# Performance work log

Hardware: AMD Instinct MI355X
Metric: run time of the kernel (lower is better)

Reference implementation:

```python
import jax, jax.numpy as jnp
import numpy as np

DIM = 256
N_PATCHES = 2048
N_HEADS = 8
BATCH = 2


def setup_inputs() -> dict:
    key = jax.random.key(0)
    ks = jax.random.split(key, 8)
    d = DIM
    s = d ** -0.5
    return {
        "x": jax.random.normal(ks[0], (BATCH, N_PATCHES, d), dtype=jnp.float32),
        # weights stored (in_features, out_features) so y = x @ W + b
        "W_qk": jax.random.normal(ks[1], (d, 2 * d), dtype=jnp.float32) * s,
        "W_v": jax.random.normal(ks[2], (d, d), dtype=jnp.float32) * s,
        "W_proj": jax.random.normal(ks[3], (d, d), dtype=jnp.float32) * s,
        "b_proj": jnp.zeros((d,), dtype=jnp.float32),
        "W_pos": jax.random.normal(ks[4], (2, N_HEADS), dtype=jnp.float32) * 0.5,
        "b_pos": jnp.zeros((N_HEADS,), dtype=jnp.float32),
        "gating": jnp.ones((N_HEADS,), dtype=jnp.float32),
    }


def reference(x, W_qk, W_v, W_proj, b_proj, W_pos, b_pos, gating):
    B, N, C = x.shape
    H = gating.shape[0]
    Dh = C // H
    scale = Dh ** -0.5

    # content attention: q @ k^T softmax
    qk = (x @ W_qk).reshape(B, N, 2, H, Dh)
    q = jnp.transpose(qk[:, :, 0], (0, 2, 1, 3))  # [B,H,N,Dh]
    k = jnp.transpose(qk[:, :, 1], (0, 2, 1, 3))
    patch_score = jax.nn.softmax(jnp.einsum("bhnd,bhmd->bhnm", q, k) * scale, axis=-1)

    # positional attention from relative indices (d, |d|) -> per-head score
    idx = jnp.arange(N, dtype=jnp.float32)
    rel = idx[:, None] - idx[None, :]                      # [N,N]
    rel_feat = jnp.stack([rel, jnp.abs(rel)], axis=-1)     # [N,N,2]
    pos = rel_feat @ W_pos + b_pos                         # [N,N,H]
    pos_score = jax.nn.softmax(jnp.transpose(pos, (2, 0, 1)), axis=-1)  # [H,N,N]

    g = jax.nn.sigmoid(gating)[None, :, None, None]        # [1,H,1,1]
    attn = (1.0 - g) * patch_score + g * pos_score[None]   # [B,H,N,N]
    attn = attn / jnp.sum(attn, axis=-1, keepdims=True)

    v = jnp.transpose((x @ W_v).reshape(B, N, H, Dh), (0, 2, 1, 3))  # [B,H,N,Dh]
    out = jnp.einsum("bhnm,bhmd->bhnd", attn, v)
    out = jnp.transpose(out, (0, 2, 1, 3)).reshape(B, N, C)
    return out @ W_proj + b_proj
```

## Files before the change

kernel.cpp:

```cpp
#include <hip/hip_runtime.h>
#include <hip/hip_bf16.h>

#define DIM 256
#define NP 2048
#define NH 8
#define BATCH 2
#define DH 32

typedef __attribute__((ext_vector_type(8))) short bshort8;
typedef __attribute__((ext_vector_type(4))) short bshort4;
typedef __attribute__((ext_vector_type(4))) float f32x4;

#define LOG2E 1.44269504f
#define QSCALE (0.17677669529663687f * LOG2E)

union U16B { uint4 u; bshort8 s8; bshort4 s4x[2]; __hip_bfloat16 h[8]; };
union U8B  { uint2 u; bshort4 s4; __hip_bfloat16 h[4]; };

__device__ __forceinline__ float fexp2(float x) { return __builtin_amdgcn_exp2f(x); }
__device__ __forceinline__ unsigned packbf(float hi, float lo) {
    return __builtin_amdgcn_perm(__float_as_uint(hi), __float_as_uint(lo), 0x07060302u);
}

__device__ __forceinline__ int lds_addr(int row, int colg) {
    return row * 256 + (((colg ^ (row & 7)) & 31) << 3);
}

__device__ __forceinline__ void gl16(const void* g, void* l) {
    __builtin_amdgcn_global_load_lds(
        (const __attribute__((address_space(1))) void*)g,
        (__attribute__((address_space(3))) void*)l, 16, 0, 0);
}

__global__ __launch_bounds__(256) void prep_kernel(
    const float* __restrict__ Wqk,
    const float* __restrict__ Wv,
    const float* __restrict__ Wproj,
    const float* __restrict__ x,
    __hip_bfloat16* __restrict__ WT,
    __hip_bfloat16* __restrict__ xb) {
    const int t = threadIdx.x;
    const int blk = blockIdx.x;
    if (blk >= 64) {
        const int base = (blk - 64) * 256 + t;
#pragma unroll
        for (int i = 0; i < 16; i++) {
            const int idx = base + i * 16384;
            float4 f = *(const float4*)(x + (size_t)idx * 4);
            U8B a;
            a.h[0] = __float2bfloat16(f.x); a.h[1] = __float2bfloat16(f.y);
            a.h[2] = __float2bfloat16(f.z); a.h[3] = __float2bfloat16(f.w);
            *(uint2*)(xb + (size_t)idx * 4) = a.u;
        }
        return;
    }
    __shared__ float ts[64][65];
    const int ct = blk >> 2, k0 = (blk & 3) * 64;
    const int c0 = ct * 64;
    const float* src; int ldw, cs0; float scl = 1.0f;
    if (ct < 8)       { src = Wqk;   ldw = 512; cs0 = c0;      if (ct < 4) scl = QSCALE; }
    else if (ct < 12) { src = Wv;    ldw = 256; cs0 = c0 - 512; }
    else              { src = Wproj; ldw = 256; cs0 = c0 - 768; }
    const int cc = t & 63, tq = t >> 6;
#pragma unroll
    for (int j = 0; j < 16; j++) {
        int kk = tq * 16 + j;
        ts[kk][cc] = src[(size_t)(k0 + kk) * ldw + cs0 + cc];
    }
    __syncthreads();
    const int kk2 = t & 63;
#pragma unroll
    for (int j = 0; j < 16; j++) {
        int cc2 = tq * 16 + j;
        WT[(size_t)(c0 + cc2) * 256 + k0 + kk2] = __float2bfloat16(ts[kk2][cc2] * scl);
    }
}

__global__ __launch_bounds__(256) void qkv_mfma(
    const __hip_bfloat16* __restrict__ xb,
    const __hip_bfloat16* __restrict__ WT,
    __hip_bfloat16* __restrict__ qT,
    __hip_bfloat16* __restrict__ k,
    __hip_bfloat16* __restrict__ vT) {
    __shared__ __align__(16) __hip_bfloat16 As[64 * 256];
    __shared__ __align__(16) __hip_bfloat16 Bs[64 * 256];
    const int t = threadIdx.x, lane = t & 63, wvid = t >> 6;
    const int l15 = lane & 15, l4 = lane >> 4;
    const int m0 = blockIdx.x * 64;
    const int nb0 = blockIdx.y * 64;
    const int nc = nb0 + wvid * 16 + l15;

    const int lrow = lane >> 5, lcg = lane & 31;
#pragma unroll
    for (int j = 0; j < 8; j++) {
        const int r0 = j * 8 + wvid * 2;
        const int row = r0 + lrow;
        const int cgs = (lcg ^ (row & 7)) & 31;
        gl16(xb + (((size_t)(m0 + row)) << 8) + cgs * 8, (char*)As + r0 * 512);
        gl16(WT + (((size_t)(nb0 + row)) << 8) + cgs * 8, (char*)Bs + r0 * 512);
    }
    __syncthreads();

    f32x4 acc[4] = {{0.f,0.f,0.f,0.f},{0.f,0.f,0.f,0.f},{0.f,0.f,0.f,0.f},{0.f,0.f,0.f,0.f}};
#pragma unroll
    for (int kk = 0; kk < 8; kk++) {
        const int colg = kk * 4 + l4;
        U16B bw; bw.u = *(const uint4*)&Bs[lds_addr(wvid * 16 + l15, colg)];
#pragma unroll
        for (int mt = 0; mt < 4; mt++) {
            U16B ax; ax.u = *(const uint4*)&As[lds_addr(mt * 16 + l15, colg)];
            acc[mt] = __builtin_amdgcn_mfma_f32_16x16x32_bf16(ax.s8, bw.s8, acc[mt], 0, 0, 0);
        }
    }

    if (nb0 < 256) {
        const int c = nc;
        const int b = m0 >> 11;
#pragma unroll
        for (int mt = 0; mt < 4; mt++) {
            int tokn = (m0 & (NP - 1)) + mt * 16 + l4 * 4;
            U8B vv;
#pragma unroll
            for (int r = 0; r < 4; r++) vv.h[r] = __float2bfloat16(acc[mt][r]);
            *(uint2*)(qT + (size_t)(b * 256 + c) * NP + tokn) = vv.u;
        }
    } else if (nb0 < 512) {
        const int c = nc - 256, h = c >> 5, d = c & 31;
#pragma unroll
        for (int mt = 0; mt < 4; mt++)
#pragma unroll
            for (int r = 0; r < 4; r++) {
                int tok = m0 + mt * 16 + l4 * 4 + r;
                int b = tok >> 11, n = tok & (NP - 1);
                k[((size_t)(b * NH + h) * NP + n) * DH + d] = __float2bfloat16(acc[mt][r]);
            }
    } else {
        const int c = nc - 512;
        const int b = m0 >> 11;
#pragma unroll
        for (int mt = 0; mt < 4; mt++) {
            int tokn = (m0 & (NP - 1)) + mt * 16 + l4 * 4;
            U8B vv;
#pragma unroll
            for (int r = 0; r < 4; r++) vv.h[r] = __float2bfloat16(acc[mt][r]);
            *(uint2*)(vT + (size_t)(b * 256 + c) * NP + tokn) = vv.u;
        }
    }
}

__global__ __launch_bounds__(512, 4) void attn_kernel(
    const __hip_bfloat16* __restrict__ qg,
    const __hip_bfloat16* __restrict__ kg,
    const __hip_bfloat16* __restrict__ vTg,
    const float* __restrict__ Wpos,
    const float* __restrict__ bpos,
    const float* __restrict__ gating,
    __hip_bfloat16* __restrict__ ao) {
    __shared__ __align__(16) __hip_bfloat16 Kt[2][2][64][40];
    __shared__ __align__(16) __hip_bfloat16 Vt[2][2][32][72];
    __shared__ float cmb[4][2][32][16];
    __shared__ float cls[4][2][16];

    const int t = threadIdx.x;
    const int lane = t & 63, wvid = t >> 6;
    const int l15 = lane & 15, l4 = lane >> 4;
    const int qt = wvid & 3, kh = wvid >> 2;
    const int bh = blockIdx.x >> 5, qb = blockIdx.x & 31;
    const int h = bh & (NH - 1), b = bh >> 3;
    const int q0 = qb * 64 + qt * 16;
    const int myq = q0 + l15;

    const int st_ = t & 255;
    const int kstart = kh * 1024;
    const __hip_bfloat16* kptr = kg + (size_t)bh * NP * DH + (size_t)(kstart + (st_ >> 2)) * DH + (st_ & 3) * 8;
    const __hip_bfloat16* vptr = vTg + ((size_t)bh * DH + (st_ >> 3)) * NP + kstart + (st_ & 7) * 8;

    const int vd = st_ >> 3, vs = st_ & 7;
    const int vc0 = ((2 * vs) & 3) * 16 + (vs >> 1) * 4;
    const int vc1 = ((2 * vs + 1) & 3) * 16 + (vs >> 1) * 4;

    uint4 kreg = *(const uint4*)kptr;
    uint4 vreg = *(const uint4*)vptr;
    *(uint4*)&Kt[kh][0][st_ >> 2][(st_ & 3) * 8] = kreg;
    *(uint2*)&Vt[kh][0][vd][vc0] = make_uint2(vreg.x, vreg.y);
    *(uint2*)&Vt[kh][0][vd][vc1] = make_uint2(vreg.z, vreg.w);

    const float w0 = Wpos[h] * LOG2E;
    const float w1 = Wpos[NH + h] * LOG2E;
    const float g = 1.0f / (1.0f + __expf(-gating[h]));
    const float nf = (float)myq;
    const float pmax = fmaxf(0.f, fmaxf((w0 + w1) * nf, (w1 - w0) * (2047.0f - nf)));
    const float npmax = -pmax;
    const float rA = fexp2(-(w0 + w1));
    const float rB = fexp2(w1 - w0);

    U16B qv;
#pragma unroll
    for (int j = 0; j < 8; j++)
        qv.h[j] = qg[((size_t)bh * DH + l4 * 8 + j) * NP + myq];

    __syncthreads();

    f32x4 os0 = {0.f,0.f,0.f,0.f}, os1 = {0.f,0.f,0.f,0.f};
    f32x4 op0 = {0.f,0.f,0.f,0.f}, op1 = {0.f,0.f,0.f,0.f};
    float ls = 0.f, lp = 0.f;

    for (int it = 0; it < 16; ++it) {
        const int cur = it & 1, nxt = cur ^ 1;

        if (it < 15) {
            kreg = *(const uint4*)(kptr + (size_t)(it + 1) * 64 * DH);
            vreg = *(const uint4*)(vptr + (it + 1) * 64);
        }

        f32x4 st4[4];
#pragma unroll
        for (int kt = 0; kt < 4; kt++) {
            U16B kf; kf.u = *(const uint4*)&Kt[kh][cur][kt * 16 + l15][l4 * 8];
            st4[kt] = __builtin_amdgcn_mfma_f32_16x16x32_bf16(
                kf.s8, qv.s8, (f32x4){0.f,0.f,0.f,0.f}, 0, 0, 0);
        }

        U16B va0, va1, vb0, vb1;
        {
            const __hip_bfloat16* v0 = &Vt[kh][cur][l15][l4 * 16];
            const __hip_bfloat16* v1 = &Vt[kh][cur][16 + l15][l4 * 16];
            va0.u = *(const uint4*)v0;
            va1.u = *(const uint4*)(v0 + 8);
            vb0.u = *(const uint4*)v1;
            vb1.u = *(const uint4*)(v1 + 8);
        }

        const int kb0 = kstart + it * 64;
#pragma unroll
        for (int kt = 0; kt < 4; kt++) {
            const bshort4 fa = (kt < 2) ? va0.s4x[kt & 1] : va1.s4x[kt & 1];
            const bshort4 fb = (kt < 2) ? vb0.s4x[kt & 1] : vb1.s4x[kt & 1];
            float es0 = fexp2(st4[kt][0]), es1 = fexp2(st4[kt][1]);
            float es2 = fexp2(st4[kt][2]), es3 = fexp2(st4[kt][3]);
            ls += (es0 + es1) + (es2 + es3);
            const float d0 = nf - (float)(kb0 + kt * 16 + l4 * 4);
            float ep0 = fexp2(fmaf(w1, fabsf(d0), fmaf(w0, d0, npmax)));
            float ep1 = ep0 * ((d0 >= 1.f) ? rA : rB);
            float ep2 = ep1 * ((d0 >= 2.f) ? rA : rB);
            float ep3 = ep2 * ((d0 >= 3.f) ? rA : rB);
            lp += (ep0 + ep1) + (ep2 + ep3);
            U8B pc, pp;
            pc.u.x = packbf(es1, es0); pc.u.y = packbf(es3, es2);
            pp.u.x = packbf(ep1, ep0); pp.u.y = packbf(ep3, ep2);
            os0 = __builtin_amdgcn_mfma_f32_16x16x16bf16_1k(fa, pc.s4, os0, 0, 0, 0);
            os1 = __builtin_amdgcn_mfma_f32_16x16x16bf16_1k(fb, pc.s4, os1, 0, 0, 0);
            op0 = __builtin_amdgcn_mfma_f32_16x16x16bf16_1k(fa, pp.s4, op0, 0, 0, 0);
            op1 = __builtin_amdgcn_mfma_f32_16x16x16bf16_1k(fb, pp.s4, op1, 0, 0, 0);
        }

        if (it < 15) {
            *(uint4*)&Kt[kh][nxt][st_ >> 2][(st_ & 3) * 8] = kreg;
            *(uint2*)&Vt[kh][nxt][vd][vc0] = make_uint2(vreg.x, vreg.y);
            *(uint2*)&Vt[kh][nxt][vd][vc1] = make_uint2(vreg.z, vreg.w);
        }
        __syncthreads();
    }

    ls += __shfl_xor(ls, 16, 64); ls += __shfl_xor(ls, 32, 64);
    lp += __shfl_xor(lp, 16, 64); lp += __shfl_xor(lp, 32, 64);

    if (kh == 1) {
#pragma unroll
        for (int r = 0; r < 4; r++) {
            cmb[qt][0][l4 * 4 + r][l15]      = os0[r];
            cmb[qt][0][16 + l4 * 4 + r][l15] = os1[r];
            cmb[qt][1][l4 * 4 + r][l15]      = op0[r];
            cmb[qt][1][16 + l4 * 4 + r][l15] = op1[r];
        }
        if (l4 == 0) { cls[qt][0][l15] = ls; cls[qt][1][l15] = lp; }
    }
    __syncthreads();
    if (kh == 0) {
        ls += cls[qt][0][l15]; lp += cls[qt][1][l15];
        const float cs = (1.0f - g) / ls;
        const float cp = g / lp;
        const size_t orow = ((size_t)b * NP + myq) * DIM + h * DH;
        U8B o0, o1;
#pragma unroll
        for (int r = 0; r < 4; r++) {
            o0.h[r] = __float2bfloat16(cs * (os0[r] + cmb[qt][0][l4 * 4 + r][l15]) +
                                       cp * (op0[r] + cmb[qt][1][l4 * 4 + r][l15]));
            o1.h[r] = __float2bfloat16(cs * (os1[r] + cmb[qt][0][16 + l4 * 4 + r][l15]) +
                                       cp * (op1[r] + cmb[qt][1][16 + l4 * 4 + r][l15]));
        }
        *(uint2*)(ao + orow + l4 * 4)      = o0.u;
        *(uint2*)(ao + orow + 16 + l4 * 4) = o1.u;
    }
}

__global__ __launch_bounds__(256) void proj_mfma(
    const __hip_bfloat16* __restrict__ ao,
    const __hip_bfloat16* __restrict__ WT,
    const float* __restrict__ bias,
    float* __restrict__ out) {
    __shared__ __align__(16) __hip_bfloat16 As[64 * 256];
    __shared__ __align__(16) __hip_bfloat16 Bs[64 * 256];
    const int t = threadIdx.x, lane = t & 63, wvid = t >> 6;
    const int l15 = lane & 15, l4 = lane >> 4;
    const int m0 = blockIdx.x * 64;
    const int nb0 = blockIdx.y * 64;
    const int nc = nb0 + wvid * 16 + l15;

    const int lrow = lane >> 5, lcg = lane & 31;
#pragma unroll
    for (int j = 0; j < 8; j++) {
        const int r0 = j * 8 + wvid * 2;
        const int row = r0 + lrow;
        const int cgs = (lcg ^ (row & 7)) & 31;
        gl16(ao + (((size_t)(m0 + row)) << 8) + cgs * 8, (char*)As + r0 * 512);
        gl16(WT + (((size_t)(768 + nb0 + row)) << 8) + cgs * 8, (char*)Bs + r0 * 512);
    }
    __syncthreads();

    f32x4 acc[4] = {{0.f,0.f,0.f,0.f},{0.f,0.f,0.f,0.f},{0.f,0.f,0.f,0.f},{0.f,0.f,0.f,0.f}};
#pragma unroll
    for (int kk = 0; kk < 8; kk++) {
        const int colg = kk * 4 + l4;
        U16B bw; bw.u = *(const uint4*)&Bs[lds_addr(wvid * 16 + l15, colg)];
#pragma unroll
        for (int mt = 0; mt < 4; mt++) {
            U16B ax; ax.u = *(const uint4*)&As[lds_addr(mt * 16 + l15, colg)];
            acc[mt] = __builtin_amdgcn_mfma_f32_16x16x32_bf16(ax.s8, bw.s8, acc[mt], 0, 0, 0);
        }
    }

    const float bb = bias[nc];
#pragma unroll
    for (int mt = 0; mt < 4; mt++)
#pragma unroll
        for (int r = 0; r < 4; r++) {
            int tok = m0 + mt * 16 + l4 * 4 + r;
            out[(size_t)tok * 256 + nc] = acc[mt][r] + bb;
        }
}

extern "C" void kernel_launch(void* const* d_in, const int* in_sizes, int n_in,
                              void* d_out, int out_size, void* d_ws, size_t ws_size,
                              hipStream_t stream) {
    const float* x      = (const float*)d_in[0];
    const float* Wqk    = (const float*)d_in[1];
    const float* Wv     = (const float*)d_in[2];
    const float* Wproj  = (const float*)d_in[3];
    const float* bproj  = (const float*)d_in[4];
    const float* Wpos   = (const float*)d_in[5];
    const float* bpos   = (const float*)d_in[6];
    const float* gating = (const float*)d_in[7];
    float* out = (float*)d_out;

    const size_t nElem = (size_t)BATCH * NP * DIM;
    char* w = (char*)d_ws;
    __hip_bfloat16* WT = (__hip_bfloat16*)w;
    __hip_bfloat16* qT = WT + 262144;
    __hip_bfloat16* k  = qT + nElem;
    __hip_bfloat16* vT = k + nElem;
    __hip_bfloat16* ao = vT + nElem;
    __hip_bfloat16* xb = ao + nElem;

    prep_kernel<<<128, 256, 0, stream>>>(Wqk, Wv, Wproj, x, WT, xb);
    qkv_mfma<<<dim3(64, 12), 256, 0, stream>>>(xb, WT, qT, k, vT);
    attn_kernel<<<BATCH * NH * (NP / 64), 512, 0, stream>>>(qT, k, vT, Wpos, bpos, gating, ao);
    proj_mfma<<<dim3(64, 4), 256, 0, stream>>>(ao, WT, bproj, out);
}
```

Measured before the change: 107.8 us.

## Fuse all four stages into one persistent kernel with grid-wide barriers

Replaces the prep, QKV GEMM, attention and projection launches with a single 512-block kernel that separates the stages using atomic-counter grid barriers, reusing one shared-memory buffer across stages. The QKV and projection GEMMs are re-tiled to 64x128 outputs with two K-chunks to fit the shared budget. This targets launch gaps and tail effects between kernels. The cost is spin-wait barrier overhead, a required memset, idle blocks during the small GEMM stages, and a deadlock risk if all 512 blocks cannot be co-resident.

```diff
diff --git a/kernel.cpp b/kernel.cpp
--- a/kernel.cpp
+++ b/kernel.cpp
@@ -21,323 +21,327 @@
 __device__ __forceinline__ unsigned packbf(float hi, float lo) {
     return __builtin_amdgcn_perm(__float_as_uint(hi), __float_as_uint(lo), 0x07060302u);
 }
-
-__device__ __forceinline__ int lds_addr(int row, int colg) {
-    return row * 256 + (((colg ^ (row & 7)) & 31) << 3);
-}
-
 __device__ __forceinline__ void gl16(const void* g, void* l) {
     __builtin_amdgcn_global_load_lds(
         (const __attribute__((address_space(1))) void*)g,
         (__attribute__((address_space(3))) void*)l, 16, 0, 0);
 }
-
-__global__ __launch_bounds__(256) void prep_kernel(
+__device__ __forceinline__ int lds_a(int row, int colg) {
+    return row * 128 + (((colg ^ (row & 7)) & 15) << 3);
+}
+
+__device__ __forceinline__ void gbar(unsigned* sem, unsigned target) {
+    __syncthreads();
+    if (threadIdx.x == 0) {
+        __threadfence();
+        __hip_atomic_fetch_add(sem, 1u, __ATOMIC_RELEASE, __HIP_MEMORY_SCOPE_AGENT);
+        while (__hip_atomic_load(sem, __ATOMIC_ACQUIRE, __HIP_MEMORY_SCOPE_AGENT) < target)
+            __builtin_amdgcn_s_sleep(8);
+        __threadfence();
+    }
+    __syncthreads();
+}
+
+struct QkvS {
+    __hip_bfloat16 As[64 * 128];
+    __hip_bfloat16 Bs[128 * 128];
+};
+struct AttnS {
+    __hip_bfloat16 Kt[2][2][64][40];
+    __hip_bfloat16 Vt[2][2][32][72];
+    float cmb[4][2][32][16];
+    float cls[4][2][16];
+};
+struct PrepS { float ts[64][65]; };
+
+__device__ __forceinline__ void gemm64x128(
+    const __hip_bfloat16* __restrict__ Ag, size_t arow0,
+    const __hip_bfloat16* __restrict__ Bg, size_t brow0,
+    QkvS& sq, int t, f32x4 acc[4])
+{
+    const int lane = t & 63, wvid = t >> 6;
+    const int l15 = lane & 15, l4 = lane >> 4;
+    const int lg = lane & 15, lr4 = lane >> 4;
+#pragma unroll
+    for (int kc = 0; kc < 2; kc++) {
+        if (kc) __syncthreads();
+#pragma unroll
+        for (int j = 0; j < 2; j++) {
+            int r = (j * 8 + wvid) * 4 + lr4;
+            int sg = lg ^ (r & 7);
+            gl16(Ag + ((arow0 + r) << 8) + kc * 128 + sg * 8,
+                 (char*)sq.As + (j * 8 + wvid) * 1024);
+        }
+#pragma unroll
+        for (int j = 0; j < 4; j++) {
+            int r = (j * 8 + wvid) * 4 + lr4;
+            int sg = lg ^ (r & 7);
+            gl16(Bg + ((brow0 + r) << 8) + kc * 128 + sg * 8,
+                 (char*)sq.Bs + (j * 8 + wvid) * 1024);
+        }
+        __syncthreads();
+#pragma unroll
+        for (int kk = 0; kk < 4; kk++) {
+            const int colg = kk * 4 + l4;
+            U16B bw; bw.u = *(const uint4*)&sq.Bs[lds_a(wvid * 16 + l15, colg)];
+#pragma unroll
+            for (int mt = 0; mt < 4; mt++) {
+                U16B ax; ax.u = *(const uint4*)&sq.As[lds_a(mt * 16 + l15, colg)];
+                acc[mt] = __builtin_amdgcn_mfma_f32_16x16x32_bf16(ax.s8, bw.s8, acc[mt], 0, 0, 0);
+            }
+        }
+    }
+}
+
+__global__ __launch_bounds__(512, 4) void fused_kernel(
+    const float* __restrict__ x,
     const float* __restrict__ Wqk,
     const float* __restrict__ Wv,
     const float* __restrict__ Wproj,
-    const float* __restrict__ x,
+    const float* __restrict__ bproj,
+    const float* __restrict__ Wpos,
+    const float* __restrict__ gating,
+    float* __restrict__ out,
     __hip_bfloat16* __restrict__ WT,
-    __hip_bfloat16* __restrict__ xb) {
+    __hip_bfloat16* __restrict__ xb,
+    __hip_bfloat16* __restrict__ qT,
+    __hip_bfloat16* __restrict__ kbuf,
+    __hip_bfloat16* __restrict__ vT,
+    __hip_bfloat16* __restrict__ ao,
+    unsigned* __restrict__ sems)
+{
+    __shared__ __align__(16) char smem[55808];
+
     const int t = threadIdx.x;
-    const int blk = blockIdx.x;
-    if (blk >= 64) {
-        const int base = (blk - 64) * 256 + t;
-#pragma unroll
-        for (int i = 0; i < 16; i++) {
-            const int idx = base + i * 16384;
+    const int bid = blockIdx.x;
+    const int lane = t & 63, wvid = t >> 6;
+    const int l15 = lane & 15, l4 = lane >> 4;
+
+    if (bid < 64) {
+        PrepS& sp = *(PrepS*)smem;
+        const int ct = bid >> 2, k0 = (bid & 3) * 64, c0 = ct * 64;
+        const float* src; int ldw, cs0; float scl = 1.0f;
+        if (ct < 8)       { src = Wqk;   ldw = 512; cs0 = c0;       if (ct < 4) scl = QSCALE; }
+        else if (ct < 12) { src = Wv;    ldw = 256; cs0 = c0 - 512; }
+        else              { src = Wproj; ldw = 256; cs0 = c0 - 768; }
+        const int cc = t & 63, tq = t >> 6;
+#pragma unroll
+        for (int j = 0; j < 8; j++) {
+            int kk = tq * 8 + j;
+            sp.ts[kk][cc] = src[(size_t)(k0 + kk) * ldw + cs0 + cc];
+        }
+        __syncthreads();
+        const int kk2 = t & 63;
+#pragma unroll
+        for (int j = 0; j < 8; j++) {
+            int cc2 = tq * 8 + j;
+            WT[(size_t)(c0 + cc2) * 256 + k0 + kk2] = __float2bfloat16(sp.ts[kk2][cc2] * scl);
+        }
+    } else {
+        const int base = (bid - 64) * 512 + t;
+        for (int idx = base; idx < 262144; idx += 229376) {
             float4 f = *(const float4*)(x + (size_t)idx * 4);
             U8B a;
             a.h[0] = __float2bfloat16(f.x); a.h[1] = __float2bfloat16(f.y);
             a.h[2] = __float2bfloat16(f.z); a.h[3] = __float2bfloat16(f.w);
             *(uint2*)(xb + (size_t)idx * 4) = a.u;
         }
-        return;
-    }
-    __shared__ float ts[64][65];
-    const int ct = blk >> 2, k0 = (blk & 3) * 64;
-    const int c0 = ct * 64;
-    const float* src; int ldw, cs0; float scl = 1.0f;
-    if (ct < 8)       { src = Wqk;   ldw = 512; cs0 = c0;      if (ct < 4) scl = QSCALE; }
-    else if (ct < 12) { src = Wv;    ldw = 256; cs0 = c0 - 512; }
-    else              { src = Wproj; ldw = 256; cs0 = c0 - 768; }
-    const int cc = t & 63, tq = t >> 6;
-#pragma unroll
-    for (int j = 0; j < 16; j++) {
-        int kk = tq * 16 + j;
-        ts[kk][cc] = src[(size_t)(k0 + kk) * ldw + cs0 + cc];
-    }
-    __syncthreads();
-    const int kk2 = t & 63;
-#pragma unroll
-    for (int j = 0; j < 16; j++) {
-        int cc2 = tq * 16 + j;
-        WT[(size_t)(c0 + cc2) * 256 + k0 + kk2] = __float2bfloat16(ts[kk2][cc2] * scl);
-    }
-}
-
-__global__ __launch_bounds__(256) void qkv_mfma(
-    const __hip_bfloat16* __restrict__ xb,
-    const __hip_bfloat16* __restrict__ WT,
-    __hip_bfloat16* __restrict__ qT,
-    __hip_bfloat16* __restrict__ k,
-    __hip_bfloat16* __restrict__ vT) {
-    __shared__ __align__(16) __hip_bfloat16 As[64 * 256];
-    __shared__ __align__(16) __hip_bfloat16 Bs[64 * 256];
-    const int t = threadIdx.x, lane = t & 63, wvid = t >> 6;
-    const int l15 = lane & 15, l4 = lane >> 4;
-    const int m0 = blockIdx.x * 64;
-    const int nb0 = blockIdx.y * 64;
-    const int nc = nb0 + wvid * 16 + l15;
-
-    const int lrow = lane >> 5, lcg = lane & 31;
-#pragma unroll
-    for (int j = 0; j < 8; j++) {
-        const int r0 = j * 8 + wvid * 2;
-        const int row = r0 + lrow;
-        const int cgs = (lcg ^ (row & 7)) & 31;
-        gl16(xb + (((size_t)(m0 + row)) << 8) + cgs * 8, (char*)As + r0 * 512);
-        gl16(WT + (((size_t)(nb0 + row)) << 8) + cgs * 8, (char*)Bs + r0 * 512);
-    }
-    __syncthreads();
-
-    f32x4 acc[4] = {{0.f,0.f,0.f,0.f},{0.f,0.f,0.f,0.f},{0.f,0.f,0.f,0.f},{0.f,0.f,0.f,0.f}};
-#pragma unroll
-    for (int kk = 0; kk < 8; kk++) {
-        const int colg = kk * 4 + l4;
-        U16B bw; bw.u = *(const uint4*)&Bs[lds_addr(wvid * 16 + l15, colg)];
-#pragma unroll
-        for (int mt = 0; mt < 4; mt++) {
-            U16B ax; ax.u = *(const uint4*)&As[lds_addr(mt * 16 + l15, colg)];
-            acc[mt] = __builtin_amdgcn_mfma_f32_16x16x32_bf16(ax.s8, bw.s8, acc[mt], 0, 0, 0);
-        }
-    }
-
-    if (nb0 < 256) {
-        const int c = nc;
-        const int b = m0 >> 11;
-#pragma unroll
-        for (int mt = 0; mt < 4; mt++) {
-            int tokn = (m0 & (NP - 1)) + mt * 16 + l4 * 4;
-            U8B vv;
-#pragma unroll
-            for (int r = 0; r < 4; r++) vv.h[r] = __float2bfloat16(acc[mt][r]);
-            *(uint2*)(qT + (size_t)(b * 256 + c) * NP + tokn) = vv.u;
-        }
-    } else if (nb0 < 512) {
-        const int c = nc - 256, h = c >> 5, d = c & 31;
+    }
+    gbar(sems + 0, 512);
+
+    if (bid < 384) {
+        QkvS& sq = *(QkvS*)smem;
+        const int ct2 = bid >> 6, rt = bid & 63;
+        const int m0 = rt * 64, nb0 = ct2 * 128;
+        f32x4 acc[4] = {{0.f,0.f,0.f,0.f},{0.f,0.f,0.f,0.f},{0.f,0.f,0.f,0.f},{0.f,0.f,0.f,0.f}};
+        gemm64x128(xb, (size_t)m0, WT, (size_t)nb0, sq, t, acc);
+
+        const int nc = nb0 + wvid * 16 + l15;
+        if (nc < 256) {
+            const int b = m0 >> 11;
+#pragma unroll
+            for (int mt = 0; mt < 4; mt++) {
+                int tokn = (m0 & (NP - 1)) + mt * 16 + l4 * 4;
+                U8B vv;
+#pragma unroll
+                for (int r = 0; r < 4; r++) vv.h[r] = __float2bfloat16(acc[mt][r]);
+                *(uint2*)(qT + (size_t)(b * 256 + nc) * NP + tokn) = vv.u;
+            }
+        } else if (nc < 512) {
+            const int c = nc - 256, h = c >> 5, d = c & 31;
+#pragma unroll
+            for (int mt = 0; mt < 4; mt++)
+#pragma unroll
+                for (int r = 0; r < 4; r++) {
+                    int tok = m0 + mt * 16 + l4 * 4 + r;
+                    int b = tok >> 11, n = tok & (NP - 1);
+                    kbuf[((size_t)(b * NH + h) * NP + n) * DH + d] = __float2bfloat16(acc[mt][r]);
+                }
+        } else {
+            const int c = nc - 512;
+            const int b = m0 >> 11;
+#pragma unroll
+            for (int mt = 0; mt < 4; mt++) {
+                int tokn = (m0 & (NP - 1)) + mt * 16 + l4 * 4;
+                U8B vv;
+#pragma unroll
+                for (int r = 0; r < 4; r++) vv.h[r] = __float2bfloat16(acc[mt][r]);
+                *(uint2*)(vT + (size_t)(b * 256 + c) * NP + tokn) = vv.u;
+            }
+        }
+    }
+    gbar(sems + 1, 512);
+
+    {
+        AttnS& sa = *(AttnS*)smem;
+        const int qt = wvid & 3, kh = wvid >> 2;
+        const int bh = bid >> 5, qb = bid & 31;
+        const int h = bh & (NH - 1), b = bh >> 3;
+        const int q0 = qb * 64 + qt * 16;
+        const int myq = q0 + l15;
+
+        const int st_ = t & 255;
+        const int kstart = kh * 1024;
+        const __hip_bfloat16* kptr = kbuf + (size_t)bh * NP * DH + (size_t)(kstart + (st_ >> 2)) * DH + (st_ & 3) * 8;
+        const __hip_bfloat16* vptr = vT + ((size_t)bh * DH + (st_ >> 3)) * NP + kstart + (st_ & 7) * 8;
+
+        const int vd = st_ >> 3, vs = st_ & 7;
+        const int vc0 = ((2 * vs) & 3) * 16 + (vs >> 1) * 4;
+        const int vc1 = ((2 * vs + 1) & 3) * 16 + (vs >> 1) * 4;
+
+        uint4 kreg = *(const uint4*)kptr;
+        uint4 vreg = *(const uint4*)vptr;
+        *(uint4*)&sa.Kt[kh][0][st_ >> 2][(st_ & 3) * 8] = kreg;
+        *(uint2*)&sa.Vt[kh][0][vd][vc0] = make_uint2(vreg.x, vreg.y);
+        *(uint2*)&sa.Vt[kh][0][vd][vc1] = make_uint2(vreg.z, vreg.w);
+
+        const float w0 = Wpos[h] * LOG2E;
+        const float w1 = Wpos[NH + h] * LOG2E;
+        const float g = 1.0f / (1.0f + __expf(-gating[h]));
+        const float nf = (float)myq;
+        const float pmax = fmaxf(0.f, fmaxf((w0 + w1) * nf, (w1 - w0) * (2047.0f - nf)));
+        const float npmax = -pmax;
+        const float rA = fexp2(-(w0 + w1));
+        const float rB = fexp2(w1 - w0);
+
+        U16B qv;
+#pragma unroll
+        for (int j = 0; j < 8; j++)
+            qv.h[j] = qT[((size_t)bh * DH + l4 * 8 + j) * NP + myq];
+
+        __syncthreads();
+
+        f32x4 os0 = {0.f,0.f,0.f,0.f}, os1 = {0.f,0.f,0.f,0.f};
+        f32x4 op0 = {0.f,0.f,0.f,0.f}, op1 = {0.f,0.f,0.f,0.f};
+        float ls = 0.f, lp = 0.f;
+
+        for (int it = 0; it < 16; ++it) {
+            const int cur = it & 1, nxt = cur ^ 1;
+
+            if (it < 15) {
+                kreg = *(const uint4*)(kptr + (size_t)(it + 1) * 64 * DH);
+                vreg = *(const uint4*)(vptr + (it + 1) * 64);
+            }
+
+            f32x4 st4[4];
+#pragma unroll
+            for (int kt = 0; kt < 4; kt++) {
+                U16B kf; kf.u = *(const uint4*)&sa.Kt[kh][cur][kt * 16 + l15][l4 * 8];
+                st4[kt] = __builtin_amdgcn_mfma_f32_16x16x32_bf16(
+                    kf.s8, qv.s8, (f32x4){0.f,0.f,0.f,0.f}, 0, 0, 0);
+            }
+
+            U16B va0, va1, vb0, vb1;
+            {
+                const __hip_bfloat16* v0 = &sa.Vt[kh][cur][l15][l4 * 16];
+                const __hip_bfloat16* v1 = &sa.Vt[kh][cur][16 + l15][l4 * 16];
+                va0.u = *(const uint4*)v0;
+                va1.u = *(const uint4*)(v0 + 8);
+                vb0.u = *(const uint4*)v1;
+                vb1.u = *(const uint4*)(v1 + 8);
+            }
+
+            const int kb0 = kstart + it * 64;
+#pragma unroll
+            for (int kt = 0; kt < 4; kt++) {
+                const bshort4 fa = (kt < 2) ? va0.s4x[kt & 1] : va1.s4x[kt & 1];
+                const bshort4 fb = (kt < 2) ? vb0.s4x[kt & 1] : vb1.s4x[kt & 1];
+                float es0 = fexp2(st4[kt][0]), es1 = fexp2(st4[kt][1]);
+                float es2 = fexp2(st4[kt][2]), es3 = fexp2(st4[kt][3]);
+                ls += (es0 + es1) + (es2 + es3);
+                const float d0 = nf - (float)(kb0 + kt * 16 + l4 * 4);
+                float ep0 = fexp2(fmaf(w1, fabsf(d0), fmaf(w0, d0, npmax)));
+                float ep1 = ep0 * ((d0 >= 1.f) ? rA : rB);
+                float ep2 = ep1 * ((d0 >= 2.f) ? rA : rB);
+                float ep3 = ep2 * ((d0 >= 3.f) ? rA : rB);
+                lp += (ep0 + ep1) + (ep2 + ep3);
+                U8B pc, pp;
+                pc.u.x = packbf(es1, es0); pc.u.y = packbf(es3, es2);
+                pp.u.x = packbf(ep1, ep0); pp.u.y = packbf(ep3, ep2);
+                os0 = __builtin_amdgcn_mfma_f32_16x16x16bf16_1k(fa, pc.s4, os0, 0, 0, 0);
+                os1 = __builtin_amdgcn_mfma_f32_16x16x16bf16_1k(fb, pc.s4, os1, 0, 0, 0);
+                op0 = __builtin_amdgcn_mfma_f32_16x16x16bf16_1k(fa, pp.s4, op0, 0, 0, 0);
+                op1 = __builtin_amdgcn_mfma_f32_16x16x16bf16_1k(fb, pp.s4, op1, 0, 0, 0);
+            }
+
+            if (it < 15) {
+                *(uint4*)&sa.Kt[kh][nxt][st_ >> 2][(st_ & 3) * 8] = kreg;
+                *(uint2*)&sa.Vt[kh][nxt][vd][vc0] = make_uint2(vreg.x, vreg.y);
+                *(uint2*)&sa.Vt[kh][nxt][vd][vc1] = make_uint2(vreg.z, vreg.w);
+            }
+            __syncthreads();
+        }
+
+        ls += __shfl_xor(ls, 16, 64); ls += __shfl_xor(ls, 32, 64);
+        lp += __shfl_xor(lp, 16, 64); lp += __shfl_xor(lp, 32, 64);
+
+        if (kh == 1) {
+#pragma unroll
+            for (int r = 0; r < 4; r++) {
+                sa.cmb[qt][0][l4 * 4 + r][l15]      = os0[r];
+                sa.cmb[qt][0][16 + l4 * 4 + r][l15] = os1[r];
+                sa.cmb[qt][1][l4 * 4 + r][l15]      = op0[r];
+                sa.cmb[qt][1][16 + l4 * 4 + r][l15] = op1[r];
+            }
+            if (l4 == 0) { sa.cls[qt][0][l15] = ls; sa.cls[qt][1][l15] = lp; }
+        }
+        __syncthreads();
+        if (kh == 0) {
+            ls += sa.cls[qt][0][l15]; lp += sa.cls[qt][1][l15];
+            const float cs = (1.0f - g) / ls;
+            const float cp = g / lp;
+            const size_t orow = ((size_t)b * NP + myq) * DIM + h * DH;
+            U8B o0, o1;
+#pragma unroll
+            for (int r = 0; r < 4; r++) {
+                o0.h[r] = __float2bfloat16(cs * (os0[r] + sa.cmb[qt][0][l4 * 4 + r][l15]) +
+                                           cp * (op0[r] + sa.cmb[qt][1][l4 * 4 + r][l15]));
+                o1.h[r] = __float2bfloat16(cs * (os1[r] + sa.cmb[qt][0][16 + l4 * 4 + r][l15]) +
+                                           cp * (op1[r] + sa.cmb[qt][1][16 + l4 * 4 + r][l15]));
+            }
+            *(uint2*)(ao + orow + l4 * 4)      = o0.u;
+            *(uint2*)(ao + orow + 16 + l4 * 4) = o1.u;
+        }
+    }
+    gbar(sems + 2, 512);
+
+    if (bid < 128) {
+        QkvS& sq = *(QkvS*)smem;
+        const int ct3 = bid >> 6, rt3 = bid & 63;
+        const int m0 = rt3 * 64, nb0 = ct3 * 128;
+        f32x4 acc[4] = {{0.f,0.f,0.f,0.f},{0.f,0.f,0.f,0.f},{0.f,0.f,0.f,0.f},{0.f,0.f,0.f,0.f}};
+        gemm64x128(ao, (size_t)m0, WT, (size_t)(768 + nb0), sq, t, acc);
+
+        const int nc = nb0 + wvid * 16 + l15;
+        const float bb = bproj[nc];
 #pragma unroll
         for (int mt = 0; mt < 4; mt++)
 #pragma unroll
             for (int r = 0; r < 4; r++) {
                 int tok = m0 + mt * 16 + l4 * 4 + r;
-                int b = tok >> 11, n = tok & (NP - 1);
-                k[((size_t)(b * NH + h) * NP + n) * DH + d] = __float2bfloat16(acc[mt][r]);
-            }
-    } else {
-        const int c = nc - 512;
-        const int b = m0 >> 11;
-#pragma unroll
-        for (int mt = 0; mt < 4; mt++) {
-            int tokn = (m0 & (NP - 1)) + mt * 16 + l4 * 4;
-            U8B vv;
-#pragma unroll
-            for (int r = 0; r < 4; r++) vv.h[r] = __float2bfloat16(acc[mt][r]);
-            *(uint2*)(vT + (size_t)(b * 256 + c) * NP + tokn) = vv.u;
-        }
-    }
-}
-
-__global__ __launch_bounds__(512, 4) void attn_kernel(
-    const __hip_bfloat16* __restrict__ qg,
-    const __hip_bfloat16* __restrict__ kg,
-    const __hip_bfloat16* __restrict__ vTg,
-    const float* __restrict__ Wpos,
-    const float* __restrict__ bpos,
-    const float* __restrict__ gating,
-    __hip_bfloat16* __restrict__ ao) {
-    __shared__ __align__(16) __hip_bfloat16 Kt[2][2][64][40];
-    __shared__ __align__(16) __hip_bfloat16 Vt[2][2][32][72];
-    __shared__ float cmb[4][2][32][16];
-    __shared__ float cls[4][2][16];
-
-    const int t = threadIdx.x;
-    const int lane = t & 63, wvid = t >> 6;
-    const int l15 = lane & 15, l4 = lane >> 4;
-    const int qt = wvid & 3, kh = wvid >> 2;
-    const int bh = blockIdx.x >> 5, qb = blockIdx.x & 31;
-    const int h = bh & (NH - 1), b = bh >> 3;
-    const int q0 = qb * 64 + qt * 16;
-    const int myq = q0 + l15;
-
-    const int st_ = t & 255;
-    const int kstart = kh * 1024;
-    const __hip_bfloat16* kptr = kg + (size_t)bh * NP * DH + (size_t)(kstart + (st_ >> 2)) * DH + (st_ & 3) * 8;
-    const __hip_bfloat16* vptr = vTg + ((size_t)bh * DH + (st_ >> 3)) * NP + kstart + (st_ & 7) * 8;
-
-    const int vd = st_ >> 3, vs = st_ & 7;
-    const int vc0 = ((2 * vs) & 3) * 16 + (vs >> 1) * 4;
-    const int vc1 = ((2 * vs + 1) & 3) * 16 + (vs >> 1) * 4;
-
-    uint4 kreg = *(const uint4*)kptr;
-    uint4 vreg = *(const uint4*)vptr;
-    *(uint4*)&Kt[kh][0][st_ >> 2][(st_ & 3) * 8] = kreg;
-    *(uint2*)&Vt[kh][0][vd][vc0] = make_uint2(vreg.x, vreg.y);
-    *(uint2*)&Vt[kh][0][vd][vc1] = make_uint2(vreg.z, vreg.w);
-
-    const float w0 = Wpos[h] * LOG2E;
-    const float w1 = Wpos[NH + h] * LOG2E;
-    const float g = 1.0f / (1.0f + __expf(-gating[h]));
-    const float nf = (float)myq;
-    const float pmax = fmaxf(0.f, fmaxf((w0 + w1) * nf, (w1 - w0) * (2047.0f - nf)));
-    const float npmax = -pmax;
-    const float rA = fexp2(-(w0 + w1));
-    const float rB = fexp2(w1 - w0);
-
-    U16B qv;
-#pragma unroll
-    for (int j = 0; j < 8; j++)
-        qv.h[j] = qg[((size_t)bh * DH + l4 * 8 + j) * NP + myq];
-
-    __syncthreads();
-
-    f32x4 os0 = {0.f,0.f,0.f,0.f}, os1 = {0.f,0.f,0.f,0.f};
-    f32x4 op0 = {0.f,0.f,0.f,0.f}, op1 = {0.f,0.f,0.f,0.f};
-    float ls = 0.f, lp = 0.f;
-
-    for (int it = 0; it < 16; ++it) {
-        const int cur = it & 1, nxt = cur ^ 1;
-
-        if (it < 15) {
-            kreg = *(const uint4*)(kptr + (size_t)(it + 1) * 64 * DH);
-            vreg = *(const uint4*)(vptr + (it + 1) * 64);
-        }
-
-        f32x4 st4[4];
-#pragma unroll
-        for (int kt = 0; kt < 4; kt++) {
-            U16B kf; kf.u = *(const uint4*)&Kt[kh][cur][kt * 16 + l15][l4 * 8];
-            st4[kt] = __builtin_amdgcn_mfma_f32_16x16x32_bf16(
-                kf.s8, qv.s8, (f32x4){0.f,0.f,0.f,0.f}, 0, 0, 0);
-        }
-
-        U16B va0, va1, vb0, vb1;
-        {
-            const __hip_bfloat16* v0 = &Vt[kh][cur][l15][l4 * 16];
-            const __hip_bfloat16* v1 = &Vt[kh][cur][16 + l15][l4 * 16];
-            va0.u = *(const uint4*)v0;
-            va1.u = *(const uint4*)(v0 + 8);
-            vb0.u = *(const uint4*)v1;
-            vb1.u = *(const uint4*)(v1 + 8);
-        }
-
-        const int kb0 = kstart + it * 64;
-#pragma unroll
-        for (int kt = 0; kt < 4; kt++) {
-            const bshort4 fa = (kt < 2) ? va0.s4x[kt & 1] : va1.s4x[kt & 1];
-            const bshort4 fb = (kt < 2) ? vb0.s4x[kt & 1] : vb1.s4x[kt & 1];
-            float es0 = fexp2(st4[kt][0]), es1 = fexp2(st4[kt][1]);
-            float es2 = fexp2(st4[kt][2]), es3 = fexp2(st4[kt][3]);
-            ls += (es0 + es1) + (es2 + es3);
-            const float d0 = nf - (float)(kb0 + kt * 16 + l4 * 4);
-            float ep0 = fexp2(fmaf(w1, fabsf(d0), fmaf(w0, d0, npmax)));
-            float ep1 = ep0 * ((d0 >= 1.f) ? rA : rB);
-            float ep2 = ep1 * ((d0 >= 2.f) ? rA : rB);
-            float ep3 = ep2 * ((d0 >= 3.f) ? rA : rB);
-            lp += (ep0 + ep1) + (ep2 + ep3);
-            U8B pc, pp;
-            pc.u.x = packbf(es1, es0); pc.u.y = packbf(es3, es2);
-            pp.u.x = packbf(ep1, ep0); pp.u.y = packbf(ep3, ep2);
-            os0 = __builtin_amdgcn_mfma_f32_16x16x16bf16_1k(fa, pc.s4, os0, 0, 0, 0);
-            os1 = __builtin_amdgcn_mfma_f32_16x16x16bf16_1k(fb, pc.s4, os1, 0, 0, 0);
-            op0 = __builtin_amdgcn_mfma_f32_16x16x16bf16_1k(fa, pp.s4, op0, 0, 0, 0);
-            op1 = __builtin_amdgcn_mfma_f32_16x16x16bf16_1k(fb, pp.s4, op1, 0, 0, 0);
-        }
-
-        if (it < 15) {
-            *(uint4*)&Kt[kh][nxt][st_ >> 2][(st_ & 3) * 8] = kreg;
-            *(uint2*)&Vt[kh][nxt][vd][vc0] = make_uint2(vreg.x, vreg.y);
-            *(uint2*)&Vt[kh][nxt][vd][vc1] = make_uint2(vreg.z, vreg.w);
-        }
-        __syncthreads();
-    }
-
-    ls += __shfl_xor(ls, 16, 64); ls += __shfl_xor(ls, 32, 64);
-    lp += __shfl_xor(lp, 16, 64); lp += __shfl_xor(lp, 32, 64);
-
-    if (kh == 1) {
-#pragma unroll
-        for (int r = 0; r < 4; r++) {
-            cmb[qt][0][l4 * 4 + r][l15]      = os0[r];
-            cmb[qt][0][16 + l4 * 4 + r][l15] = os1[r];
-            cmb[qt][1][l4 * 4 + r][l15]      = op0[r];
-            cmb[qt][1][16 + l4 * 4 + r][l15] = op1[r];
-        }
-        if (l4 == 0) { cls[qt][0][l15] = ls; cls[qt][1][l15] = lp; }
-    }
-    __syncthreads();
-    if (kh == 0) {
-        ls += cls[qt][0][l15]; lp += cls[qt][1][l15];
-        const float cs = (1.0f - g) / ls;
-        const float cp = g / lp;
-        const size_t orow = ((size_t)b * NP + myq) * DIM + h * DH;
-        U8B o0, o1;
-#pragma unroll
-        for (int r = 0; r < 4; r++) {
-            o0.h[r] = __float2bfloat16(cs * (os0[r] + cmb[qt][0][l4 * 4 + r][l15]) +
-                                       cp * (op0[r] + cmb[qt][1][l4 * 4 + r][l15]));
-            o1.h[r] = __float2bfloat16(cs * (os1[r] + cmb[qt][0][16 + l4 * 4 + r][l15]) +
-                                       cp * (op1[r] + cmb[qt][1][16 + l4 * 4 + r][l15]));
-        }
-        *(uint2*)(ao + orow + l4 * 4)      = o0.u;
-        *(uint2*)(ao + orow + 16 + l4 * 4) = o1.u;
-    }
-}
-
-__global__ __launch_bounds__(256) void proj_mfma(
-    const __hip_bfloat16* __restrict__ ao,
-    const __hip_bfloat16* __restrict__ WT,
-    const float* __restrict__ bias,
-    float* __restrict__ out) {
-    __shared__ __align__(16) __hip_bfloat16 As[64 * 256];
-    __shared__ __align__(16) __hip_bfloat16 Bs[64 * 256];
-    const int t = threadIdx.x, lane = t & 63, wvid = t >> 6;
-    const int l15 = lane & 15, l4 = lane >> 4;
-    const int m0 = blockIdx.x * 64;
-    const int nb0 = blockIdx.y * 64;
-    const int nc = nb0 + wvid * 16 + l15;
-
-    const int lrow = lane >> 5, lcg = lane & 31;
-#pragma unroll
-    for (int j = 0; j < 8; j++) {
-        const int r0 = j * 8 + wvid * 2;
-        const int row = r0 + lrow;
-        const int cgs = (lcg ^ (row & 7)) & 31;
-        gl16(ao + (((size_t)(m0 + row)) << 8) + cgs * 8, (char*)As + r0 * 512);
-        gl16(WT + (((size_t)(768 + nb0 + row)) << 8) + cgs * 8, (char*)Bs + r0 * 512);
-    }
-    __syncthreads();
-
-    f32x4 acc[4] = {{0.f,0.f,0.f,0.f},{0.f,0.f,0.f,0.f},{0.f,0.f,0.f,0.f},{0.f,0.f,0.f,0.f}};
-#pragma unroll
-    for (int kk = 0; kk < 8; kk++) {
-        const int colg = kk * 4 + l4;
-        U16B bw; bw.u = *(const uint4*)&Bs[lds_addr(wvid * 16 + l15, colg)];
-#pragma unroll
-        for (int mt = 0; mt < 4; mt++) {
-            U16B ax; ax.u = *(const uint4*)&As[lds_addr(mt * 16 + l15, colg)];
-            acc[mt] = __builtin_amdgcn_mfma_f32_16x16x32_bf16(ax.s8, bw.s8, acc[mt], 0, 0, 0);
-        }
-    }
-
-    const float bb = bias[nc];
-#pragma unroll
-    for (int mt = 0; mt < 4; mt++)
-#pragma unroll
-        for (int r = 0; r < 4; r++) {
-            int tok = m0 + mt * 16 + l4 * 4 + r;
-            out[(size_t)tok * 256 + nc] = acc[mt][r] + bb;
-        }
+                out[(size_t)tok * 256 + nc] = acc[mt][r] + bb;
+            }
+    }
 }
 
 extern "C" void kernel_launch(void* const* d_in, const int* in_sizes, int n_in,
@@ -349,7 +353,6 @@
     const float* Wproj  = (const float*)d_in[3];
     const float* bproj  = (const float*)d_in[4];
     const float* Wpos   = (const float*)d_in[5];
-    const float* bpos   = (const float*)d_in[6];
     const float* gating = (const float*)d_in[7];
     float* out = (float*)d_out;
 
@@ -357,13 +360,14 @@
     char* w = (char*)d_ws;
     __hip_bfloat16* WT = (__hip_bfloat16*)w;
     __hip_bfloat16* qT = WT + 262144;
-    __hip_bfloat16* k  = qT + nElem;
-    __hip_bfloat16* vT = k + nElem;
+    __hip_bfloat16* kb = qT + nElem;
+    __hip_bfloat16* vT = kb + nElem;
     __hip_bfloat16* ao = vT + nElem;
     __hip_bfloat16* xb = ao + nElem;
-
-    prep_kernel<<<128, 256, 0, stream>>>(Wqk, Wv, Wproj, x, WT, xb);
-    qkv_mfma<<<dim3(64, 12), 256, 0, stream>>>(xb, WT, qT, k, vT);
-    attn_kernel<<<BATCH * NH * (NP / 64), 512, 0, stream>>>(qT, k, vT, Wpos, bpos, gating, ao);
-    proj_mfma<<<dim3(64, 4), 256, 0, stream>>>(ao, WT, bproj, out);
-}
+    unsigned* sems = (unsigned*)(w + (16u << 20));
+
+    hipMemsetAsync(sems, 0, 256, stream);
+
+    fused_kernel<<<512, 512, 0, stream>>>(x, Wqk, Wv, Wproj, bproj, Wpos, gating,
+                                          out, WT, xb, qT, kb, vT, ao, sems);
+}
```

New measurement: 342.3 us. 218% more time.
